# Kernel tuning notes

Hardware: AMD Instinct MI355X
Metric: run time of the kernel (lower is better)

The kernel has to match this reference:

```python
import jax, jax.numpy as jnp
import numpy as np

KINEMATIC_CHAIN = [[0,2,5,8,11],[0,1,4,7,10],[0,3,6,9,12,15],[9,14,17,19,21],[9,13,16,18,20]]
_paths = [c[1:] for c in KINEMATIC_CHAIN]
SEG_S = np.array([p[i] for p in _paths for i in range(len(p)-1)])      # [16] segment start joints
SEG_E = np.array([p[i+1] for p in _paths for i in range(len(p)-1)])    # [16] segment end joints
PATH_ID = np.array([k for k, p in enumerate(_paths) for _ in range(len(p)-1)])
N_PATHS = len(_paths)
P_ONEHOT = (PATH_ID[:, None] == np.arange(N_PATHS)[None, :]).astype(np.float32)  # [16,5]


def _safe_normalize(v):
    ss = jnp.sum(v * v, axis=-1, keepdims=True)
    return jnp.where(ss > 0, v / jnp.sqrt(jnp.where(ss > 0, ss, 1.0)), 0.0)


def _gli_pairwise(s1, e1, s2, e2):
    # all inputs broadcast to [..., 3]; returns Gauss linking integral per segment pair
    r13, r14 = s2 - s1, e2 - s1
    r23, r24 = s2 - e1, e2 - e1
    r12, r34 = e1 - s1, e2 - s2
    f0 = _safe_normalize(jnp.cross(r13, r14))
    f1 = _safe_normalize(jnp.cross(r14, r24))
    f2 = _safe_normalize(jnp.cross(r24, r23))
    f3 = _safe_normalize(jnp.cross(r23, r13))
    def asin_dot(a, b):
        return jnp.arcsin(jnp.clip(jnp.sum(a * b, -1), -1.0, 1.0))
    total = asin_dot(f0, f1) + asin_dot(f1, f2) + asin_dot(f2, f3) + asin_dot(f3, f0)
    sign = jnp.sum(jnp.cross(r34, r12) * r13, -1)
    mult = jnp.where(sign <= 0, -1.0, 1.0)
    return mult * total / (4.0 * jnp.pi)


def _bbox_xz(m):
    x, z = m[..., 0], m[..., 2]
    return x.min(-1), x.max(-1), z.min(-1), z.max(-1)


def setup_inputs() -> dict:
    key = jax.random.key(0)
    k1, k2 = jax.random.split(key)
    B, F, J = 64, 240, 22
    motion1 = jax.random.normal(k1, (B, F, J, 3), dtype=jnp.float32)
    motion2 = jax.random.normal(k2, (B, F, J, 3), dtype=jnp.float32)
    return {"motion1": motion1, "motion2": motion2}


def reference(motion1, motion2):
    B, F = motion1.shape[0], motion1.shape[1]
    P = jnp.asarray(P_ONEHOT, motion1.dtype)
    # gather all 16 skeleton segments, broadcast to 16x16 segment pairs
    s1 = motion1[..., SEG_S, :][..., :, None, :]   # [B,F,16,1,3]
    e1 = motion1[..., SEG_E, :][..., :, None, :]
    s2 = motion2[..., SEG_S, :][..., None, :, :]   # [B,F,1,16,3]
    e2 = motion2[..., SEG_E, :][..., None, :, :]
    gli_seg = _gli_pairwise(s1, e1, s2, e2)        # [B,F,16,16]
    # sum segment-pair GLIs into path-pair blocks -> [B,F,5,5]
    gli_pose = jnp.einsum('bfmn,mi,nj->bfij', gli_seg, P, P)

    # xz bounding-box overlap per frame, then dilate by 1 frame (window start-1..end+1)
    nx1, xx1, nz1, xz1 = _bbox_xz(motion1)
    nx2, xx2, nz2, xz2 = _bbox_xz(motion2)
    flag = (xx1 >= nx2) & (xx2 >= nx1) & (xz1 >= nz2) & (xz2 >= nz1)   # [B,F]
    pad = jnp.zeros_like(flag[:, :1])
    mask = flag | jnp.concatenate([flag[:, 1:], pad], 1) | jnp.concatenate([pad, flag[:, :-1]], 1)
    gli_motion = gli_pose * mask[..., None, None].astype(gli_pose.dtype)

    vel = jnp.abs(gli_motion[:, 1:] - gli_motion[:, :-1]).reshape(B, F - 1, -1)
    return vel.max(-1)
```

## Files before the change

### kernel.cpp

```cpp
#include <hip/hip_runtime.h>
#include <math.h>

#define BB 64
#define FF 240
#define NJ 22
#define NFRM (BB * FF)

#define PK8(a0,a1,a2,a3,a4,a5,a6,a7) \
  (  (unsigned long long)(a0)        | ((unsigned long long)(a1) << 5)  \
   | ((unsigned long long)(a2) << 10)| ((unsigned long long)(a3) << 15) \
   | ((unsigned long long)(a4) << 20)| ((unsigned long long)(a5) << 25) \
   | ((unsigned long long)(a6) << 30)| ((unsigned long long)(a7) << 35) )
static constexpr unsigned long long SEG_S_LO = PK8(2,5,8,1,4,7,3,6);
static constexpr unsigned long long SEG_S_HI = PK8(9,12,14,17,19,13,16,18);
static constexpr unsigned long long SEG_E_LO = PK8(5,8,11,4,7,10,6,9);
static constexpr unsigned long long SEG_E_HI = PK8(12,15,17,19,21,16,18,20);
static constexpr unsigned PO_PK = 0u | (3u<<5) | (6u<<10) | (10u<<15) | (13u<<20);
static constexpr unsigned PC_PK = 3u | (3u<<5) | (4u<<10) | (3u<<15)  | (3u<<20);

struct F3 { float x, y, z; };
__device__ __forceinline__ F3 sub(F3 a, F3 b){ return {a.x-b.x, a.y-b.y, a.z-b.z}; }
__device__ __forceinline__ F3 crs(F3 a, F3 b){
    return {fmaf(a.y, b.z, -a.z*b.y), fmaf(a.z, b.x, -a.x*b.z), fmaf(a.x, b.y, -a.y*b.x)};
}
__device__ __forceinline__ float dt(F3 a, F3 b){ return fmaf(a.x, b.x, fmaf(a.y, b.y, a.z*b.z)); }
__device__ __forceinline__ float clamp1(float d){ return fminf(fmaxf(d, -1.0f), 1.0f); }

__device__ __forceinline__ float asin_fast(float d){
    float ax = fabsf(d);
    float p = fmaf(fmaf(fmaf(-0.0187293f, ax, 0.0742610f), ax, -0.2121144f), ax, 1.5707288f);
    float r = 1.57079632679f - __builtin_amdgcn_sqrtf(1.0f - ax) * p;
    return copysignf(r, d);
}

__global__ void __launch_bounds__(256, 4) k_main(const float* __restrict__ m1,
                                                 const float* __restrict__ m2,
                                                 float* __restrict__ gp,
                                                 int* __restrict__ flags){
    __shared__ __align__(8) float seg[4][2][2][16][6];
    __shared__ float g[4][2][256];
    __shared__ float ext[4][2][8];
    int tid = threadIdx.x;
    int w = tid >> 6, lane = tid & 63;
    int fr0 = blockIdx.x * 8 + w * 2;

    {
        int m = lane & 15, mot = (lane >> 4) & 1, f = lane >> 5;
        unsigned long long ps = (m < 8) ? SEG_S_LO : SEG_S_HI;
        unsigned long long pe = (m < 8) ? SEG_E_LO : SEG_E_HI;
        int sh = (m & 7) * 5;
        int js = (int)((ps >> sh) & 31);
        int je = (int)((pe >> sh) & 31);
        const float* P = (mot ? m2 : m1) + (size_t)(fr0 + f) * 66;
        float* d = &seg[w][f][mot][m][0];
        d[0] = P[js*3]; d[1] = P[js*3+1]; d[2] = P[js*3+2];
        d[3] = P[je*3]; d[4] = P[je*3+1]; d[5] = P[je*3+2];
    }
    if (lane < 16){
        int f = lane >> 3;
        int sel = lane & 7;
        int mot = sel >> 2;
        int c = sel & 2;
        bool mx = sel & 1;
        const float* P = (mot ? m2 : m1) + (size_t)(fr0 + f) * 66;
        float a = 1e30f;
        #pragma unroll
        for (int j = 0; j < NJ; ++j){
            float v = P[j*3 + c];
            a = fminf(a, mx ? -v : v);
        }
        ext[w][f][sel] = mx ? -a : a;
    }
    __syncthreads();

    int n = lane & 15, q = lane >> 4;
    F3 s2f[2], e2f[2];
    #pragma unroll
    for (int f = 0; f < 2; ++f){
        const float* B = &seg[w][f][1][n][0];
        float2 b0 = *(const float2*)(B+0);
        float2 b1 = *(const float2*)(B+2);
        float2 b2 = *(const float2*)(B+4);
        s2f[f] = {b0.x, b0.y, b1.x};
        e2f[f] = {b1.y, b2.x, b2.y};
    }

    float rd01[2][4], rd12[2][4], rd23[2][4], rd30[2][4];
    float q01[2][4], q12[2][4], q23[2][4], q30[2][4];
    float sg[2][4];
    #pragma unroll
    for (int f = 0; f < 2; ++f){
        F3 s2 = s2f[f], e2 = e2f[f];
        #pragma unroll
        for (int k = 0; k < 4; ++k){
            int m = q + 4 * k;
            const float* A = &seg[w][f][0][m][0];
            float2 a0 = *(const float2*)(A+0);
            float2 a1 = *(const float2*)(A+2);
            float2 a2 = *(const float2*)(A+4);
            F3 s1 = {a0.x, a0.y, a1.x};
            F3 e1 = {a1.y, a2.x, a2.y};
            F3 r13 = sub(s2, s1), r14 = sub(e2, s1);
            F3 r23 = sub(s2, e1), r24 = sub(e2, e1);
            F3 f0 = crs(r13, r14);
            F3 f1 = crs(r14, r24);
            F3 f2 = crs(r24, r23);
            F3 f3 = crs(r23, r13);
            float ss0 = dt(f0,f0), ss1 = dt(f1,f1), ss2 = dt(f2,f2), ss3 = dt(f3,f3);
            rd01[f][k] = dt(f0,f1); rd12[f][k] = dt(f1,f2);
            rd23[f][k] = dt(f2,f3); rd30[f][k] = dt(f3,f0);
            q01[f][k] = ss0*ss1; q12[f][k] = ss1*ss2;
            q23[f][k] = ss2*ss3; q30[f][k] = ss3*ss0;
            sg[f][k] = dt(f3, r14);
        }
    }
    float i01[2][4], i12[2][4], i23[2][4], i30[2][4];
    #pragma unroll
    for (int f = 0; f < 2; ++f)
    #pragma unroll
    for (int k = 0; k < 4; ++k){
        i01[f][k] = rsqrtf(fmaxf(q01[f][k], 1e-30f));
        i12[f][k] = rsqrtf(fmaxf(q12[f][k], 1e-30f));
        i23[f][k] = rsqrtf(fmaxf(q23[f][k], 1e-30f));
        i30[f][k] = rsqrtf(fmaxf(q30[f][k], 1e-30f));
    }
    #pragma unroll
    for (int f = 0; f < 2; ++f)
    #pragma unroll
    for (int k = 0; k < 4; ++k){
        float t = asin_fast(clamp1(rd01[f][k] * i01[f][k]))
                + asin_fast(clamp1(rd12[f][k] * i12[f][k]))
                + asin_fast(clamp1(rd23[f][k] * i23[f][k]))
                + asin_fast(clamp1(rd30[f][k] * i30[f][k]));
        float r = (sg[f][k] >= 0.0f ? -t : t) * 0.07957747154594767f;
        g[w][f][(k << 6) | lane] = r;
    }
    __syncthreads();

    if (lane < 50){
        int f = lane >= 25 ? 1 : 0;
        int pp = lane - f * 25;
        int i = pp / 5, j = pp - i * 5;
        int poi = (int)((PO_PK >> (i*5)) & 31), pci = (int)((PC_PK >> (i*5)) & 31);
        int poj = (int)((PO_PK >> (j*5)) & 31), pcj = (int)((PC_PK >> (j*5)) & 31);
        float s = 0.0f;
        for (int a = 0; a < pci; ++a)
            for (int b = 0; b < pcj; ++b)
                s += g[w][f][(poi + a) * 16 + (poj + b)];
        int fr = fr0 + f;
        int bb = fr / FF, ff = fr - bb * FF;
        gp[((size_t)bb * 25 + pp) * FF + ff] = s;
    } else if (lane < 52){
        int f = lane - 50;
        const float* e = ext[w][f];
        flags[fr0 + f] = (e[1] >= e[4] && e[5] >= e[0] &&
                          e[3] >= e[6] && e[7] >= e[2]) ? 1 : 0;
    }
}

__global__ void __launch_bounds__(256) k_vel(const float* __restrict__ gp,
                                             const int* __restrict__ flags,
                                             float* __restrict__ out){
    int b = blockIdx.x;
    int f = threadIdx.x;
    if (f >= FF - 1) return;
    const int* fl = flags + b * FF;

    int v0 = fl[f] | fl[f + 1];
    if (f > 0) v0 |= fl[f - 1];
    float mk0 = v0 ? 1.0f : 0.0f;

    int v1 = fl[f] | fl[f + 1];
    if (f + 2 < FF) v1 |= fl[f + 2];
    float mk1 = v1 ? 1.0f : 0.0f;

    const float* gb = gp + (size_t)b * 25 * FF + f;
    float mx = 0.0f;
    #pragma unroll
    for (int p = 0; p < 25; ++p){
        float g0 = gb[p * FF];
        float g1 = gb[p * FF + 1];
        float d = fabsf(g1 * mk1 - g0 * mk0);
        mx = fmaxf(mx, d);
    }
    out[b * (FF - 1) + f] = mx;
}

extern "C" void kernel_launch(void* const* d_in, const int* in_sizes, int n_in,
                              void* d_out, int out_size, void* d_ws, size_t ws_size,
                              hipStream_t stream) {
    const float* m1 = (const float*)d_in[0];
    const float* m2 = (const float*)d_in[1];
    float* gp    = (float*)d_ws;
    int*   flags = (int*)((char*)d_ws + (size_t)BB * 25 * FF * 4);
    float* out = (float*)d_out;

    k_main<<<NFRM / 8, 256, 0, stream>>>(m1, m2, gp, flags);
    k_vel<<<BB, 256, 0, stream>>>(gp, flags, out);
}
```

Baseline: 78.55 us.

## Pack two frames into float2 vectors for packed FMA and stage raw joints in LDS

The main kernel now loads each frame's full joint arrays into LDS with coalesced float2 copies, replacing the gather of segment endpoints. Both frames a wave handles are packed into 2-wide float vectors so the cross products, dot products and asin polynomial can map to packed FP32 instructions. The bounding-box pass now reads from LDS instead of global memory. The launch-bounds occupancy hint is dropped, which may raise register use and lower occupancy, and the segment-index decode now happens inside the compute loop.

```diff
diff --git a/kernel.cpp b/kernel.cpp
--- a/kernel.cpp
+++ b/kernel.cpp
@@ -18,51 +18,65 @@
 static constexpr unsigned PO_PK = 0u | (3u<<5) | (6u<<10) | (10u<<15) | (13u<<20);
 static constexpr unsigned PC_PK = 3u | (3u<<5) | (4u<<10) | (3u<<15)  | (3u<<20);
 
-struct F3 { float x, y, z; };
-__device__ __forceinline__ F3 sub(F3 a, F3 b){ return {a.x-b.x, a.y-b.y, a.z-b.z}; }
-__device__ __forceinline__ F3 crs(F3 a, F3 b){
-    return {fmaf(a.y, b.z, -a.z*b.y), fmaf(a.z, b.x, -a.x*b.z), fmaf(a.x, b.y, -a.y*b.x)};
-}
-__device__ __forceinline__ float dt(F3 a, F3 b){ return fmaf(a.x, b.x, fmaf(a.y, b.y, a.z*b.z)); }
-__device__ __forceinline__ float clamp1(float d){ return fminf(fmaxf(d, -1.0f), 1.0f); }
-
-__device__ __forceinline__ float asin_fast(float d){
-    float ax = fabsf(d);
-    float p = fmaf(fmaf(fmaf(-0.0187293f, ax, 0.0742610f), ax, -0.2121144f), ax, 1.5707288f);
-    float r = 1.57079632679f - __builtin_amdgcn_sqrtf(1.0f - ax) * p;
-    return copysignf(r, d);
-}
-
-__global__ void __launch_bounds__(256, 4) k_main(const float* __restrict__ m1,
-                                                 const float* __restrict__ m2,
-                                                 float* __restrict__ gp,
-                                                 int* __restrict__ flags){
-    __shared__ __align__(8) float seg[4][2][2][16][6];
+__device__ __forceinline__ int seg_start(int m){
+    unsigned long long p = (m < 8) ? SEG_S_LO : SEG_S_HI;
+    return (int)((p >> ((m & 7) * 5)) & 31);
+}
+__device__ __forceinline__ int seg_end(int m){
+    unsigned long long p = (m < 8) ? SEG_E_LO : SEG_E_HI;
+    return (int)((p >> ((m & 7) * 5)) & 31);
+}
+
+typedef float v2 __attribute__((ext_vector_type(2)));
+__device__ __forceinline__ v2 vset(float a){ v2 r; r.x = a; r.y = a; return r; }
+__device__ __forceinline__ v2 vfma(v2 a, v2 b, v2 c){ return __builtin_elementwise_fma(a, b, c); }
+
+struct V3p { v2 x, y, z; };
+__device__ __forceinline__ V3p subp(V3p a, V3p b){ return {a.x-b.x, a.y-b.y, a.z-b.z}; }
+__device__ __forceinline__ V3p crsp(V3p a, V3p b){
+    return { vfma(a.y, b.z, -(a.z*b.y)), vfma(a.z, b.x, -(a.x*b.z)), vfma(a.x, b.y, -(a.y*b.x)) };
+}
+__device__ __forceinline__ v2 dtp(V3p a, V3p b){ return vfma(a.x, b.x, vfma(a.y, b.y, a.z*b.z)); }
+__device__ __forceinline__ v2 clamp1p(v2 d){
+    return __builtin_elementwise_min(__builtin_elementwise_max(d, vset(-1.0f)), vset(1.0f));
+}
+__device__ __forceinline__ v2 asin_fast2(v2 d){
+    v2 ax = __builtin_elementwise_abs(d);
+    v2 p = vfma(vfma(vfma(vset(-0.0187293f), ax, vset(0.0742610f)), ax, vset(-0.2121144f)),
+                ax, vset(1.5707288f));
+    v2 om = vset(1.0f) - ax;
+    v2 s; s.x = __builtin_amdgcn_sqrtf(om.x); s.y = __builtin_amdgcn_sqrtf(om.y);
+    v2 r = vset(1.57079632679f) - s * p;
+    return __builtin_elementwise_copysign(r, d);
+}
+
+__global__ void __launch_bounds__(256) k_main(const float* __restrict__ m1,
+                                              const float* __restrict__ m2,
+                                              float* __restrict__ gp,
+                                              int* __restrict__ flags){
+    __shared__ __align__(8) float pts[4][2][136];
     __shared__ float g[4][2][256];
     __shared__ float ext[4][2][8];
     int tid = threadIdx.x;
     int w = tid >> 6, lane = tid & 63;
     int fr0 = blockIdx.x * 8 + w * 2;
 
-    {
-        int m = lane & 15, mot = (lane >> 4) & 1, f = lane >> 5;
-        unsigned long long ps = (m < 8) ? SEG_S_LO : SEG_S_HI;
-        unsigned long long pe = (m < 8) ? SEG_E_LO : SEG_E_HI;
-        int sh = (m & 7) * 5;
-        int js = (int)((ps >> sh) & 31);
-        int je = (int)((pe >> sh) & 31);
-        const float* P = (mot ? m2 : m1) + (size_t)(fr0 + f) * 66;
-        float* d = &seg[w][f][mot][m][0];
-        d[0] = P[js*3]; d[1] = P[js*3+1]; d[2] = P[js*3+2];
-        d[3] = P[je*3]; d[4] = P[je*3+1]; d[5] = P[je*3+2];
-    }
+    const float2* gs1 = (const float2*)(m1 + (size_t)fr0 * 66);
+    const float2* gs2 = (const float2*)(m2 + (size_t)fr0 * 66);
+    for (int u = lane; u < 132; u += 64){
+        bool a = u < 66;
+        int v = a ? u : u - 66;
+        ((float2*)pts[w][a ? 0 : 1])[v] = (a ? gs1 : gs2)[v];
+    }
+    __syncthreads();
+
     if (lane < 16){
         int f = lane >> 3;
         int sel = lane & 7;
         int mot = sel >> 2;
         int c = sel & 2;
         bool mx = sel & 1;
-        const float* P = (mot ? m2 : m1) + (size_t)(fr0 + f) * 66;
+        const float* P = &pts[w][mot][f * 66];
         float a = 1e30f;
         #pragma unroll
         for (int j = 0; j < NJ; ++j){
@@ -71,69 +85,65 @@
         }
         ext[w][f][sel] = mx ? -a : a;
     }
-    __syncthreads();
 
     int n = lane & 15, q = lane >> 4;
-    F3 s2f[2], e2f[2];
-    #pragma unroll
-    for (int f = 0; f < 2; ++f){
-        const float* B = &seg[w][f][1][n][0];
-        float2 b0 = *(const float2*)(B+0);
-        float2 b1 = *(const float2*)(B+2);
-        float2 b2 = *(const float2*)(B+4);
-        s2f[f] = {b0.x, b0.y, b1.x};
-        e2f[f] = {b1.y, b2.x, b2.y};
-    }
-
-    float rd01[2][4], rd12[2][4], rd23[2][4], rd30[2][4];
-    float q01[2][4], q12[2][4], q23[2][4], q30[2][4];
-    float sg[2][4];
-    #pragma unroll
-    for (int f = 0; f < 2; ++f){
-        F3 s2 = s2f[f], e2 = e2f[f];
-        #pragma unroll
-        for (int k = 0; k < 4; ++k){
-            int m = q + 4 * k;
-            const float* A = &seg[w][f][0][m][0];
-            float2 a0 = *(const float2*)(A+0);
-            float2 a1 = *(const float2*)(A+2);
-            float2 a2 = *(const float2*)(A+4);
-            F3 s1 = {a0.x, a0.y, a1.x};
-            F3 e1 = {a1.y, a2.x, a2.y};
-            F3 r13 = sub(s2, s1), r14 = sub(e2, s1);
-            F3 r23 = sub(s2, e1), r24 = sub(e2, e1);
-            F3 f0 = crs(r13, r14);
-            F3 f1 = crs(r14, r24);
-            F3 f2 = crs(r24, r23);
-            F3 f3 = crs(r23, r13);
-            float ss0 = dt(f0,f0), ss1 = dt(f1,f1), ss2 = dt(f2,f2), ss3 = dt(f3,f3);
-            rd01[f][k] = dt(f0,f1); rd12[f][k] = dt(f1,f2);
-            rd23[f][k] = dt(f2,f3); rd30[f][k] = dt(f3,f0);
-            q01[f][k] = ss0*ss1; q12[f][k] = ss1*ss2;
-            q23[f][k] = ss2*ss3; q30[f][k] = ss3*ss0;
-            sg[f][k] = dt(f3, r14);
-        }
-    }
-    float i01[2][4], i12[2][4], i23[2][4], i30[2][4];
-    #pragma unroll
-    for (int f = 0; f < 2; ++f)
+    const float* P1 = pts[w][0];
+    const float* P2 = pts[w][1];
+    int js2 = seg_start(n) * 3, je2 = seg_end(n) * 3;
+    V3p s2 = { v2{P2[js2  ], P2[66+js2  ]},
+               v2{P2[js2+1], P2[66+js2+1]},
+               v2{P2[js2+2], P2[66+js2+2]} };
+    V3p e2 = { v2{P2[je2  ], P2[66+je2  ]},
+               v2{P2[je2+1], P2[66+je2+1]},
+               v2{P2[je2+2], P2[66+je2+2]} };
+
+    v2 rd01[4], rd12[4], rd23[4], rd30[4];
+    v2 q01[4], q12[4], q23[4], q30[4];
+    v2 sg[4];
     #pragma unroll
     for (int k = 0; k < 4; ++k){
-        i01[f][k] = rsqrtf(fmaxf(q01[f][k], 1e-30f));
-        i12[f][k] = rsqrtf(fmaxf(q12[f][k], 1e-30f));
-        i23[f][k] = rsqrtf(fmaxf(q23[f][k], 1e-30f));
-        i30[f][k] = rsqrtf(fmaxf(q30[f][k], 1e-30f));
-    }
-    #pragma unroll
-    for (int f = 0; f < 2; ++f)
+        int m = q + 4 * k;
+        int js1 = seg_start(m) * 3, je1 = seg_end(m) * 3;
+        V3p s1 = { v2{P1[js1  ], P1[66+js1  ]},
+                   v2{P1[js1+1], P1[66+js1+1]},
+                   v2{P1[js1+2], P1[66+js1+2]} };
+        V3p e1 = { v2{P1[je1  ], P1[66+je1  ]},
+                   v2{P1[je1+1], P1[66+je1+1]},
+                   v2{P1[je1+2], P1[66+je1+2]} };
+        V3p r13 = subp(s2, s1), r14 = subp(e2, s1);
+        V3p r23 = subp(s2, e1), r24 = subp(e2, e1);
+        V3p f0 = crsp(r13, r14);
+        V3p f1 = crsp(r14, r24);
+        V3p f2 = crsp(r24, r23);
+        V3p f3 = crsp(r23, r13);
+        v2 ss0 = dtp(f0,f0), ss1 = dtp(f1,f1), ss2 = dtp(f2,f2), ss3 = dtp(f3,f3);
+        rd01[k] = dtp(f0,f1); rd12[k] = dtp(f1,f2);
+        rd23[k] = dtp(f2,f3); rd30[k] = dtp(f3,f0);
+        q01[k] = ss0*ss1; q12[k] = ss1*ss2; q23[k] = ss2*ss3; q30[k] = ss3*ss0;
+        sg[k] = dtp(f3, r14);
+    }
+    v2 i01[4], i12[4], i23[4], i30[4];
     #pragma unroll
     for (int k = 0; k < 4; ++k){
-        float t = asin_fast(clamp1(rd01[f][k] * i01[f][k]))
-                + asin_fast(clamp1(rd12[f][k] * i12[f][k]))
-                + asin_fast(clamp1(rd23[f][k] * i23[f][k]))
-                + asin_fast(clamp1(rd30[f][k] * i30[f][k]));
-        float r = (sg[f][k] >= 0.0f ? -t : t) * 0.07957747154594767f;
-        g[w][f][(k << 6) | lane] = r;
+        i01[k].x = rsqrtf(fmaxf(q01[k].x, 1e-30f));
+        i01[k].y = rsqrtf(fmaxf(q01[k].y, 1e-30f));
+        i12[k].x = rsqrtf(fmaxf(q12[k].x, 1e-30f));
+        i12[k].y = rsqrtf(fmaxf(q12[k].y, 1e-30f));
+        i23[k].x = rsqrtf(fmaxf(q23[k].x, 1e-30f));
+        i23[k].y = rsqrtf(fmaxf(q23[k].y, 1e-30f));
+        i30[k].x = rsqrtf(fmaxf(q30[k].x, 1e-30f));
+        i30[k].y = rsqrtf(fmaxf(q30[k].y, 1e-30f));
+    }
+    #pragma unroll
+    for (int k = 0; k < 4; ++k){
+        v2 t = asin_fast2(clamp1p(rd01[k] * i01[k]))
+             + asin_fast2(clamp1p(rd12[k] * i12[k]))
+             + asin_fast2(clamp1p(rd23[k] * i23[k]))
+             + asin_fast2(clamp1p(rd30[k] * i30[k]));
+        float r0 = (sg[k].x >= 0.0f ? -t.x : t.x) * 0.07957747154594767f;
+        float r1 = (sg[k].y >= 0.0f ? -t.y : t.y) * 0.07957747154594767f;
+        g[w][0][(k << 6) | lane] = r0;
+        g[w][1][(k << 6) | lane] = r1;
     }
     __syncthreads();
 
```

After: 75.88 us, median of 2. 1.04x faster.
